# Kernel optimization log

Hardware: AMD Instinct MI355X
Metric: run time of the kernel (lower is better)

## Reference

```python
import jax, jax.numpy as jnp
import numpy as np

N_NODES = 100000
N_EDGES = 1600000
IN_FEATS = 256
H_FEATS = 256
NUM_CLASSES = 64


def setup_inputs() -> dict:
    key = jax.random.key(0)
    ks = jax.random.split(key, 7)
    x = jax.random.normal(ks[0], (N_NODES, IN_FEATS), dtype=jnp.float32)
    src = jax.random.randint(ks[1], (N_EDGES,), 0, N_NODES, dtype=jnp.int64)
    dst = jax.random.randint(ks[2], (N_EDGES,), 0, N_NODES, dtype=jnp.int64)
    W = jax.random.normal(ks[3], (IN_FEATS, H_FEATS), dtype=jnp.float32) / np.sqrt(IN_FEATS)
    b = jax.random.normal(ks[4], (H_FEATS,), dtype=jnp.float32) * 0.01
    W2 = jax.random.normal(ks[5], (H_FEATS, NUM_CLASSES), dtype=jnp.float32) / np.sqrt(H_FEATS)
    b2 = jax.random.normal(ks[6], (NUM_CLASSES,), dtype=jnp.float32) * 0.01
    return {"x": x, "src": src, "dst": dst, "W": W, "b": b, "W2": W2, "b2": b2}


def reference(x, src, dst, W, b, W2, b2):
    N = x.shape[0]
    ones_e = jnp.ones(src.shape[0], dtype=x.dtype)
    # DGL GraphConv norm='both': D_out^{-1/2} on source side, D_in^{-1/2} on dest side
    out_deg = jnp.clip(jax.ops.segment_sum(ones_e, src, num_segments=N), 1.0)
    in_deg = jnp.clip(jax.ops.segment_sum(ones_e, dst, num_segments=N), 1.0)
    h = x * jax.lax.rsqrt(out_deg)[:, None]
    h = h @ W  # [N, h_feats]
    agg = jax.ops.segment_sum(h[src], dst, num_segments=N)  # sparse neighbor aggregation
    agg = agg * jax.lax.rsqrt(in_deg)[:, None] + b
    h = jax.nn.relu(agg)
    pooled = h.mean(axis=0)  # [h_feats]
    logits = pooled @ W2 + b2  # [num_classes]
    return jax.nn.softmax(logits, axis=0)
```

## Files before the change

### kernel.cpp

```cpp
#include <hip/hip_runtime.h>
#include <hip/hip_bf16.h>
#include <hip/hip_fp8.h>

#define M_N  100000
#define N_E  1600000
#define FEAT 256
#define NCLS 64
#define SCAN_NB ((M_N + 255) / 256)

typedef __attribute__((ext_vector_type(8))) short bf16x8;
typedef __attribute__((ext_vector_type(8))) ushort u16x8;
typedef __attribute__((ext_vector_type(4))) float f32x4;
typedef unsigned char uchar;

__device__ __forceinline__ ushort f2bf(float f) {
    __hip_bfloat16 h = __float2bfloat16(f);
    return __builtin_bit_cast(ushort, h);
}
__device__ __forceinline__ void load_lds16(const void* g, void* l) {
    __builtin_amdgcn_global_load_lds(
        (const __attribute__((address_space(1))) void*)g,
        (__attribute__((address_space(3))) void*)l, 16, 0, 0);
}
__device__ __forceinline__ float fp8f(uint b) {
    b &= 0xffu;
    uint bits = ((b & 0x80u) << 24) | (((b & 0x7fu) << 20) + 0x3C000000u);
    return __uint_as_float(bits);
}

__global__ void deg_kernel(const int* __restrict__ src, const int* __restrict__ dst,
                           int* __restrict__ cnt_out, int* __restrict__ cnt_in, int nE) {
    int i = blockIdx.x * blockDim.x + threadIdx.x;
    int stride = gridDim.x * blockDim.x;
    for (int e = i; e < nE; e += stride) {
        atomicAdd(&cnt_out[src[e]], 1);
        atomicAdd(&cnt_in[dst[e]], 1);
    }
}

__global__ __launch_bounds__(256) void scanA_kernel(const int* __restrict__ cnt_in,
                                                    int* __restrict__ bsum) {
    __shared__ int sh[256];
    int t = threadIdx.x;
    int i = blockIdx.x * 256 + t;
    sh[t] = (i < M_N) ? cnt_in[i] : 0;
    __syncthreads();
#pragma unroll
    for (int o = 128; o > 0; o >>= 1) {
        if (t < o) sh[t] += sh[t + o];
        __syncthreads();
    }
    if (t == 0) bsum[blockIdx.x] = sh[0];
}

__global__ __launch_bounds__(512) void scanB_kernel(int* __restrict__ bsum) {
    __shared__ int sh[512];
    int t = threadIdx.x;
    int v = (t < SCAN_NB) ? bsum[t] : 0;
    sh[t] = v;
    __syncthreads();
    for (int o = 1; o < 512; o <<= 1) {
        int u = (t >= o) ? sh[t - o] : 0;
        __syncthreads();
        sh[t] += u;
        __syncthreads();
    }
    if (t < SCAN_NB) bsum[t] = sh[t] - v;
}

__global__ __launch_bounds__(256) void scanC_kernel(
    const int* __restrict__ cnt_in, const int* __restrict__ cnt_out,
    const int* __restrict__ bsum, int* __restrict__ row_start,
    int* __restrict__ cursor, float* __restrict__ rs_out) {
    __shared__ int sh[256];
    int t = threadIdx.x;
    int i = blockIdx.x * 256 + t;
    int v = (i < M_N) ? cnt_in[i] : 0;
    sh[t] = v;
    __syncthreads();
    for (int o = 1; o < 256; o <<= 1) {
        int u = (t >= o) ? sh[t - o] : 0;
        __syncthreads();
        sh[t] += u;
        __syncthreads();
    }
    int base = bsum[blockIdx.x];
    int excl = base + sh[t] - v;
    if (i < M_N) {
        row_start[i] = excl;
        cursor[i]    = excl;
        int co = cnt_out[i]; if (co < 1) co = 1;
        rs_out[i] = rsqrtf((float)co);
        if (i == M_N - 1) row_start[M_N] = excl + v;
    }
}

__global__ void bucket_kernel(const int* __restrict__ src, const int* __restrict__ dst,
                              int* __restrict__ cursor, int* __restrict__ csr_src, int nE) {
    int i = blockIdx.x * blockDim.x + threadIdx.x;
    int stride = gridDim.x * blockDim.x;
    for (int e = i; e < nE; e += stride) {
        int pos = atomicAdd(&cursor[dst[e]], 1);
        csr_src[pos] = src[e];
    }
}

__global__ void wt_kernel(const float* __restrict__ W, ushort* __restrict__ Wt) {
    int i = blockIdx.x * blockDim.x + threadIdx.x;
    if (i < FEAT * FEAT) {
        int k = i >> 8, n = i & 255;
        Wt[n * FEAT + k] = f2bf(W[i]);
    }
}

__global__ __launch_bounds__(256) void gemm_xw_kernel(
    const float* __restrict__ x, const float* __restrict__ rs_out,
    const ushort* __restrict__ Wt, uchar* __restrict__ xw8) {
    __shared__ ushort As[128 * 32];
    __shared__ ushort Bs[128 * 32];
    const int tid  = threadIdx.x;
    const int lane = tid & 63;
    const int w    = tid >> 6;
    const int wr   = w >> 1, wc = w & 1;
    const int m0   = blockIdx.x * 128;
    const int n0   = blockIdx.y * 128;

    const int ar = tid >> 1;
    const int ah = tid & 1;
    int arow = m0 + ar; if (arow >= M_N) arow = M_N - 1;
    const float rsA = rs_out[arow];
    const float* xrow = x + (size_t)arow * FEAT + ah * 16;

    const int lr = lane >> 2;
    const int lb = (lane & 3) * 16;

    f32x4 acc[4][4];
#pragma unroll
    for (int i = 0; i < 4; ++i)
#pragma unroll
        for (int j = 0; j < 4; ++j) {
            acc[i][j][0] = 0.f; acc[i][j][1] = 0.f;
            acc[i][j][2] = 0.f; acc[i][j][3] = 0.f;
        }

    for (int k0 = 0; k0 < FEAT; k0 += 32) {
        __syncthreads();
#pragma unroll
        for (int j = 0; j < 2; ++j) {
            const int seg = (w * 2 + j) * 1024;
            int row = (seg >> 6) + lr;
            load_lds16((const char*)Wt + (size_t)(n0 + row) * 512 + k0 * 2 + lb,
                       (char*)Bs + seg);
        }
        float4 f0 = *(const float4*)(xrow + k0 + 0);
        float4 f1 = *(const float4*)(xrow + k0 + 4);
        float4 f2 = *(const float4*)(xrow + k0 + 8);
        float4 f3 = *(const float4*)(xrow + k0 + 12);
        u16x8 lo, hi;
        lo[0] = f2bf(f0.x * rsA); lo[1] = f2bf(f0.y * rsA);
        lo[2] = f2bf(f0.z * rsA); lo[3] = f2bf(f0.w * rsA);
        lo[4] = f2bf(f1.x * rsA); lo[5] = f2bf(f1.y * rsA);
        lo[6] = f2bf(f1.z * rsA); lo[7] = f2bf(f1.w * rsA);
        hi[0] = f2bf(f2.x * rsA); hi[1] = f2bf(f2.y * rsA);
        hi[2] = f2bf(f2.z * rsA); hi[3] = f2bf(f2.w * rsA);
        hi[4] = f2bf(f3.x * rsA); hi[5] = f2bf(f3.y * rsA);
        hi[6] = f2bf(f3.z * rsA); hi[7] = f2bf(f3.w * rsA);
        *(u16x8*)((char*)As + ar * 64 + ah * 32)      = lo;
        *(u16x8*)((char*)As + ar * 64 + ah * 32 + 16) = hi;
        __syncthreads();

        bf16x8 a[4], b[4];
#pragma unroll
        for (int mi = 0; mi < 4; ++mi) {
            int row = wr * 64 + mi * 16 + (lane & 15);
            a[mi] = *(const bf16x8*)((const char*)As + row * 64 + (lane >> 4) * 16);
        }
#pragma unroll
        for (int ni = 0; ni < 4; ++ni) {
            int n = wc * 64 + ni * 16 + (lane & 15);
            b[ni] = *(const bf16x8*)((const char*)Bs + n * 64 + (lane >> 4) * 16);
        }
#pragma unroll
        for (int mi = 0; mi < 4; ++mi)
#pragma unroll
            for (int ni = 0; ni < 4; ++ni)
                acc[mi][ni] = __builtin_amdgcn_mfma_f32_16x16x32_bf16(
                    a[mi], b[ni], acc[mi][ni], 0, 0, 0);
    }

#pragma unroll
    for (int mi = 0; mi < 4; ++mi) {
        int rbase = m0 + wr * 64 + mi * 16 + (lane >> 4) * 4;
#pragma unroll
        for (int ni = 0; ni < 4; ++ni) {
            int col = n0 + wc * 64 + ni * 16 + (lane & 15);
#pragma unroll
            for (int j = 0; j < 4; ++j) {
                int r = rbase + j;
                if (r < M_N) {
                    __hip_fp8_e4m3 q(acc[mi][ni][j]);
                    xw8[(size_t)r * FEAT + col] = q.__x;
                }
            }
        }
    }
}

__global__ __launch_bounds__(256) void gather_pool_kernel(
    const uchar* __restrict__ xw8, const int* __restrict__ csr_src,
    const int* __restrict__ row_start, const float* __restrict__ bias,
    float* __restrict__ pooled, int d_lo, int d_hi) {
    __shared__ float pool_lds[FEAT];
    int tid = threadIdx.x;
    pool_lds[tid] = 0.0f;
    __syncthreads();
    int lane = tid & 63;
    int wave = tid >> 6;
    int gw = blockIdx.x * 4 + wave;
    int nw = gridDim.x * 4;
    float b0 = bias[lane * 4 + 0], b1 = bias[lane * 4 + 1];
    float b2 = bias[lane * 4 + 2], b3 = bias[lane * 4 + 3];
    float p0 = 0.f, p1 = 0.f, p2 = 0.f, p3 = 0.f;

    for (int d = d_lo + gw; d < d_hi; d += nw) {
        int e0 = row_start[d], e1 = row_start[d + 1];
        float s0 = 0.f, s1 = 0.f, s2 = 0.f, s3 = 0.f;
        int e = e0;
        for (; e + 3 < e1; e += 4) {
            int ia = csr_src[e], ib = csr_src[e + 1];
            int ic = csr_src[e + 2], id = csr_src[e + 3];
            uint ua = *(const uint*)(xw8 + (size_t)ia * FEAT + lane * 4);
            uint ub = *(const uint*)(xw8 + (size_t)ib * FEAT + lane * 4);
            uint uc = *(const uint*)(xw8 + (size_t)ic * FEAT + lane * 4);
            uint ud = *(const uint*)(xw8 + (size_t)id * FEAT + lane * 4);
            s0 += (fp8f(ua) + fp8f(ub)) + (fp8f(uc) + fp8f(ud));
            s1 += (fp8f(ua >> 8) + fp8f(ub >> 8)) + (fp8f(uc >> 8) + fp8f(ud >> 8));
            s2 += (fp8f(ua >> 16) + fp8f(ub >> 16)) + (fp8f(uc >> 16) + fp8f(ud >> 16));
            s3 += (fp8f(ua >> 24) + fp8f(ub >> 24)) + (fp8f(uc >> 24) + fp8f(ud >> 24));
        }
        for (; e < e1; ++e) {
            int ia = csr_src[e];
            uint ua = *(const uint*)(xw8 + (size_t)ia * FEAT + lane * 4);
            s0 += fp8f(ua); s1 += fp8f(ua >> 8);
            s2 += fp8f(ua >> 16); s3 += fp8f(ua >> 24);
        }
        float ri = rsqrtf(fmaxf((float)(e1 - e0), 1.0f));
        p0 += fmaxf(s0 * ri + b0, 0.f);
        p1 += fmaxf(s1 * ri + b1, 0.f);
        p2 += fmaxf(s2 * ri + b2, 0.f);
        p3 += fmaxf(s3 * ri + b3, 0.f);
    }
    atomicAdd(&pool_lds[lane * 4 + 0], p0);
    atomicAdd(&pool_lds[lane * 4 + 1], p1);
    atomicAdd(&pool_lds[lane * 4 + 2], p2);
    atomicAdd(&pool_lds[lane * 4 + 3], p3);
    __syncthreads();
    atomicAdd(&pooled[tid], pool_lds[tid]);
}

__global__ void final_kernel(const float* __restrict__ pooled, const float* __restrict__ W2,
                             const float* __restrict__ b2, float* __restrict__ out) {
    int c = threadIdx.x;
    const float invN = 1.0f / (float)M_N;
    float acc = 0.0f;
    for (int f = 0; f < FEAT; ++f) acc += pooled[f] * W2[f * NCLS + c];
    acc = acc * invN + b2[c];
    float m = acc;
#pragma unroll
    for (int o = 32; o > 0; o >>= 1) m = fmaxf(m, __shfl_xor(m, o));
    float e = expf(acc - m);
    float s = e;
#pragma unroll
    for (int o = 32; o > 0; o >>= 1) s += __shfl_xor(s, o);
    out[c] = e / s;
}

extern "C" void kernel_launch(void* const* d_in, const int* in_sizes, int n_in,
                              void* d_out, int out_size, void* d_ws, size_t ws_size,
                              hipStream_t stream) {
    const float* x   = (const float*)d_in[0];
    const int*   src = (const int*)d_in[1];
    const int*   dst = (const int*)d_in[2];
    const float* W   = (const float*)d_in[3];
    const float* b   = (const float*)d_in[4];
    const float* W2  = (const float*)d_in[5];
    const float* b2  = (const float*)d_in[6];
    float* out = (float*)d_out;

    char* p = (char*)d_ws;
    uchar*  xw8      = (uchar*)p;   p += (size_t)M_N * FEAT;
    ushort* Wt       = (ushort*)p;  p += (size_t)FEAT * FEAT * 2;
    int*    cnt_out  = (int*)p;     p += (size_t)M_N * 4;
    int*    cnt_in   = (int*)p;     p += (size_t)M_N * 4;
    float*  pooled   = (float*)p;   p += 1024;
    int*    row_start= (int*)p;     p += ((size_t)M_N + 8) * 4;
    int*    cursor   = (int*)p;     p += (size_t)M_N * 4;
    float*  rs_out   = (float*)p;   p += (size_t)M_N * 4;
    int*    bsum     = (int*)p;     p += 2048;
    int*    csr_src  = (int*)p;     p += (size_t)N_E * 4;

    hipMemsetAsync(cnt_out, 0, (size_t)(2 * M_N) * 4 + 1024, stream);

    deg_kernel<<<1024, 256, 0, stream>>>(src, dst, cnt_out, cnt_in, N_E);
    scanA_kernel<<<SCAN_NB, 256, 0, stream>>>(cnt_in, bsum);
    scanB_kernel<<<1, 512, 0, stream>>>(bsum);
    scanC_kernel<<<SCAN_NB, 256, 0, stream>>>(cnt_in, cnt_out, bsum,
                                              row_start, cursor, rs_out);
    bucket_kernel<<<1024, 256, 0, stream>>>(src, dst, cursor, csr_src, N_E);
    wt_kernel<<<(FEAT * FEAT + 255) / 256, 256, 0, stream>>>(W, Wt);
    gemm_xw_kernel<<<dim3((M_N + 127) / 128, 2), 256, 0, stream>>>(x, rs_out, Wt, xw8);
    gather_pool_kernel<<<1024, 256, 0, stream>>>(xw8, csr_src, row_start, b, pooled,
                                                 0, M_N / 2);
    gather_pool_kernel<<<1024, 256, 0, stream>>>(xw8, csr_src, row_start, b, pooled,
                                                 M_N / 2, M_N);
    final_kernel<<<1, 64, 0, stream>>>(pooled, W2, b2, out);
}
```

Measured before the change: 622.1 us.

## Build CSR via two-level bucket sort and stage GEMM fp8 output through LDS

Replaces the per-node in-degree histogram, three-kernel scan and global-atomic bucketing with a coarse 128-node bucket histogram kept in LDS, a single-block scan, a pass that scatters (src,dst) pairs into coarse buckets, and a per-bucket local counting sort in LDS that writes csr_src and row_start. This cuts heavily contended global atomics on 100k counters and the scattered csr writes, at the cost of an extra 12.8MB pairs buffer round trip. Separately, the GEMM epilogue stages fp8 results in a 16KB LDS tile so each row is written with coalesced 16-byte stores instead of scattered byte stores, which raises the GEMM's LDS use.

```diff
diff --git a/kernel.cpp b/kernel.cpp
--- a/kernel.cpp
+++ b/kernel.cpp
@@ -6,7 +6,8 @@
 #define N_E  1600000
 #define FEAT 256
 #define NCLS 64
-#define SCAN_NB ((M_N + 255) / 256)
+#define BKT_SH 7
+#define NBKT ((M_N + 127) >> BKT_SH)
 
 typedef __attribute__((ext_vector_type(8))) short bf16x8;
 typedef __attribute__((ext_vector_type(8))) ushort u16x8;
@@ -28,80 +29,104 @@
     return __uint_as_float(bits);
 }
 
-__global__ void deg_kernel(const int* __restrict__ src, const int* __restrict__ dst,
-                           int* __restrict__ cnt_out, int* __restrict__ cnt_in, int nE) {
+__global__ __launch_bounds__(256) void hist_kernel(
+    const int* __restrict__ src, const int* __restrict__ dst,
+    int* __restrict__ cnt_out, int* __restrict__ coarse_cnt, int nE) {
+    __shared__ int lh[NBKT];
+    int tid = threadIdx.x;
+    for (int i = tid; i < NBKT; i += 256) lh[i] = 0;
+    __syncthreads();
+    int i = blockIdx.x * 256 + tid;
+    int stride = gridDim.x * 256;
+    for (int e = i; e < nE; e += stride) {
+        atomicAdd(&cnt_out[src[e]], 1);
+        atomicAdd(&lh[dst[e] >> BKT_SH], 1);
+    }
+    __syncthreads();
+    for (int i2 = tid; i2 < NBKT; i2 += 256) {
+        int v = lh[i2];
+        if (v) atomicAdd(&coarse_cnt[i2], v);
+    }
+}
+
+__global__ __launch_bounds__(1024) void cscan_kernel(
+    const int* __restrict__ coarse_cnt, int* __restrict__ cbase,
+    int* __restrict__ ccur) {
+    __shared__ int sh[1024];
+    int t = threadIdx.x;
+    int v = (t < NBKT) ? coarse_cnt[t] : 0;
+    sh[t] = v;
+    __syncthreads();
+    for (int o = 1; o < 1024; o <<= 1) {
+        int u = (t >= o) ? sh[t - o] : 0;
+        __syncthreads();
+        sh[t] += u;
+        __syncthreads();
+    }
+    if (t < NBKT) {
+        int excl = sh[t] - v;
+        cbase[t] = excl;
+        ccur[t * 16] = excl;
+    }
+    if (t == 0) cbase[NBKT] = N_E;
+}
+
+__global__ void rs_kernel(const int* __restrict__ cnt_out,
+                          float* __restrict__ rs_out, int n) {
+    int i = blockIdx.x * blockDim.x + threadIdx.x;
+    if (i < n) {
+        int co = cnt_out[i]; if (co < 1) co = 1;
+        rs_out[i] = rsqrtf((float)co);
+    }
+}
+
+__global__ void pair_kernel(const int* __restrict__ src, const int* __restrict__ dst,
+                            int* __restrict__ ccur, int2* __restrict__ pairs, int nE) {
     int i = blockIdx.x * blockDim.x + threadIdx.x;
     int stride = gridDim.x * blockDim.x;
     for (int e = i; e < nE; e += stride) {
-        atomicAdd(&cnt_out[src[e]], 1);
-        atomicAdd(&cnt_in[dst[e]], 1);
-    }
-}
-
-__global__ __launch_bounds__(256) void scanA_kernel(const int* __restrict__ cnt_in,
-                                                    int* __restrict__ bsum) {
-    __shared__ int sh[256];
+        int s = src[e], d = dst[e];
+        int pos = atomicAdd(&ccur[(d >> BKT_SH) * 16], 1);
+        pairs[pos] = make_int2(s, d);
+    }
+}
+
+__global__ __launch_bounds__(256) void lsort_kernel(
+    const int2* __restrict__ pairs, const int* __restrict__ cbase,
+    int* __restrict__ csr_src, int* __restrict__ row_start) {
+    __shared__ int cnt[128];
+    __shared__ int loc[128];
+    int b = blockIdx.x;
     int t = threadIdx.x;
-    int i = blockIdx.x * 256 + t;
-    sh[t] = (i < M_N) ? cnt_in[i] : 0;
-    __syncthreads();
-#pragma unroll
-    for (int o = 128; o > 0; o >>= 1) {
-        if (t < o) sh[t] += sh[t + o];
-        __syncthreads();
-    }
-    if (t == 0) bsum[blockIdx.x] = sh[0];
-}
-
-__global__ __launch_bounds__(512) void scanB_kernel(int* __restrict__ bsum) {
-    __shared__ int sh[512];
-    int t = threadIdx.x;
-    int v = (t < SCAN_NB) ? bsum[t] : 0;
-    sh[t] = v;
-    __syncthreads();
-    for (int o = 1; o < 512; o <<= 1) {
-        int u = (t >= o) ? sh[t - o] : 0;
-        __syncthreads();
-        sh[t] += u;
-        __syncthreads();
-    }
-    if (t < SCAN_NB) bsum[t] = sh[t] - v;
-}
-
-__global__ __launch_bounds__(256) void scanC_kernel(
-    const int* __restrict__ cnt_in, const int* __restrict__ cnt_out,
-    const int* __restrict__ bsum, int* __restrict__ row_start,
-    int* __restrict__ cursor, float* __restrict__ rs_out) {
-    __shared__ int sh[256];
-    int t = threadIdx.x;
-    int i = blockIdx.x * 256 + t;
-    int v = (i < M_N) ? cnt_in[i] : 0;
-    sh[t] = v;
-    __syncthreads();
-    for (int o = 1; o < 256; o <<= 1) {
-        int u = (t >= o) ? sh[t - o] : 0;
-        __syncthreads();
-        sh[t] += u;
-        __syncthreads();
-    }
-    int base = bsum[blockIdx.x];
-    int excl = base + sh[t] - v;
-    if (i < M_N) {
-        row_start[i] = excl;
-        cursor[i]    = excl;
-        int co = cnt_out[i]; if (co < 1) co = 1;
-        rs_out[i] = rsqrtf((float)co);
-        if (i == M_N - 1) row_start[M_N] = excl + v;
-    }
-}
-
-__global__ void bucket_kernel(const int* __restrict__ src, const int* __restrict__ dst,
-                              int* __restrict__ cursor, int* __restrict__ csr_src, int nE) {
-    int i = blockIdx.x * blockDim.x + threadIdx.x;
-    int stride = gridDim.x * blockDim.x;
-    for (int e = i; e < nE; e += stride) {
-        int pos = atomicAdd(&cursor[dst[e]], 1);
-        csr_src[pos] = src[e];
+    int lo = cbase[b], hi = cbase[b + 1];
+    int n = hi - lo;
+    int d0 = b << BKT_SH;
+    if (t < 128) cnt[t] = 0;
+    __syncthreads();
+    for (int i = t; i < n; i += 256) {
+        int d = pairs[lo + i].y - d0;
+        atomicAdd(&cnt[d], 1);
+    }
+    __syncthreads();
+    int v = (t < 128) ? cnt[t] : 0;
+    for (int o = 1; o < 128; o <<= 1) {
+        int u = (t >= o && t < 128) ? cnt[t - o] : 0;
+        __syncthreads();
+        if (t < 128) cnt[t] += u;
+        __syncthreads();
+    }
+    if (t < 128) {
+        int excl = cnt[t] - v;
+        loc[t] = lo + excl;
+        int d = d0 + t;
+        if (d < M_N) row_start[d] = lo + excl;
+    }
+    if (b == NBKT - 1 && t == 0) row_start[M_N] = N_E;
+    __syncthreads();
+    for (int i = t; i < n; i += 256) {
+        int2 p = pairs[lo + i];
+        int off = atomicAdd(&loc[p.y - d0], 1);
+        csr_src[off] = p.x;
     }
 }
 
@@ -118,6 +143,7 @@
     const ushort* __restrict__ Wt, uchar* __restrict__ xw8) {
     __shared__ ushort As[128 * 32];
     __shared__ ushort Bs[128 * 32];
+    __shared__ uchar  Cs[128 * 128];
     const int tid  = threadIdx.x;
     const int lane = tid & 63;
     const int w    = tid >> 6;
@@ -177,8 +203,8 @@
         }
 #pragma unroll
         for (int ni = 0; ni < 4; ++ni) {
-            int n = wc * 64 + ni * 16 + (lane & 15);
-            b[ni] = *(const bf16x8*)((const char*)Bs + n * 64 + (lane >> 4) * 16);
+            int nn = wc * 64 + ni * 16 + (lane & 15);
+            b[ni] = *(const bf16x8*)((const char*)Bs + nn * 64 + (lane >> 4) * 16);
         }
 #pragma unroll
         for (int mi = 0; mi < 4; ++mi)
@@ -190,18 +216,26 @@
 
 #pragma unroll
     for (int mi = 0; mi < 4; ++mi) {
-        int rbase = m0 + wr * 64 + mi * 16 + (lane >> 4) * 4;
+        int rl = wr * 64 + mi * 16 + (lane >> 4) * 4;
 #pragma unroll
         for (int ni = 0; ni < 4; ++ni) {
-            int col = n0 + wc * 64 + ni * 16 + (lane & 15);
+            int cl = wc * 64 + ni * 16 + (lane & 15);
 #pragma unroll
             for (int j = 0; j < 4; ++j) {
-                int r = rbase + j;
-                if (r < M_N) {
-                    __hip_fp8_e4m3 q(acc[mi][ni][j]);
-                    xw8[(size_t)r * FEAT + col] = q.__x;
-                }
+                __hip_fp8_e4m3 q(acc[mi][ni][j]);
+                Cs[(rl + j) * 128 + cl] = q.__x;
             }
+        }
+    }
+    __syncthreads();
+    {
+        int row = tid >> 1, half = tid & 1;
+        int gr = m0 + row;
+        if (gr < M_N) {
+            const f32x4* s = (const f32x4*)(Cs + row * 128 + half * 64);
+            f32x4* dgl = (f32x4*)(xw8 + (size_t)gr * FEAT + n0 + half * 64);
+            dgl[0] = s[0]; dgl[1] = s[1];
+            dgl[2] = s[2]; dgl[3] = s[3];
         }
     }
 }
@@ -291,22 +325,22 @@
     uchar*  xw8      = (uchar*)p;   p += (size_t)M_N * FEAT;
     ushort* Wt       = (ushort*)p;  p += (size_t)FEAT * FEAT * 2;
     int*    cnt_out  = (int*)p;     p += (size_t)M_N * 4;
-    int*    cnt_in   = (int*)p;     p += (size_t)M_N * 4;
+    int*    coarse   = (int*)p;     p += (size_t)NBKT * 4 + 8;
     float*  pooled   = (float*)p;   p += 1024;
+    int*    cbase    = (int*)p;     p += ((size_t)NBKT + 4) * 4;
+    int*    ccur     = (int*)p;     p += (size_t)NBKT * 64;
     int*    row_start= (int*)p;     p += ((size_t)M_N + 8) * 4;
-    int*    cursor   = (int*)p;     p += (size_t)M_N * 4;
     float*  rs_out   = (float*)p;   p += (size_t)M_N * 4;
-    int*    bsum     = (int*)p;     p += 2048;
+    int2*   pairs    = (int2*)p;    p += (size_t)N_E * 8;
     int*    csr_src  = (int*)p;     p += (size_t)N_E * 4;
 
-    hipMemsetAsync(cnt_out, 0, (size_t)(2 * M_N) * 4 + 1024, stream);
-
-    deg_kernel<<<1024, 256, 0, stream>>>(src, dst, cnt_out, cnt_in, N_E);
-    scanA_kernel<<<SCAN_NB, 256, 0, stream>>>(cnt_in, bsum);
-    scanB_kernel<<<1, 512, 0, stream>>>(bsum);
-    scanC_kernel<<<SCAN_NB, 256, 0, stream>>>(cnt_in, cnt_out, bsum,
-                                              row_start, cursor, rs_out);
-    bucket_kernel<<<1024, 256, 0, stream>>>(src, dst, cursor, csr_src, N_E);
+    hipMemsetAsync(cnt_out, 0, (size_t)M_N * 4 + (size_t)NBKT * 4 + 8 + 1024, stream);
+
+    hist_kernel<<<512, 256, 0, stream>>>(src, dst, cnt_out, coarse, N_E);
+    cscan_kernel<<<1, 1024, 0, stream>>>(coarse, cbase, ccur);
+    rs_kernel<<<(M_N + 255) / 256, 256, 0, stream>>>(cnt_out, rs_out, M_N);
+    pair_kernel<<<1024, 256, 0, stream>>>(src, dst, ccur, pairs, N_E);
+    lsort_kernel<<<NBKT, 256, 0, stream>>>(pairs, cbase, csr_src, row_start);
     wt_kernel<<<(FEAT * FEAT + 255) / 256, 256, 0, stream>>>(W, Wt);
     gemm_xw_kernel<<<dim3((M_N + 127) / 128, 2), 256, 0, stream>>>(x, rs_out, Wt, xw8);
     gather_pool_kernel<<<1024, 256, 0, stream>>>(xw8, csr_src, row_start, b, pooled,
```

Measured after the change: 543.4 us. 12.6% less time.
